# Performance work log

Hardware: AMD Instinct MI355X
Metric: run time of the kernel (lower is better)

The kernel has to match this reference:

```python
import jax, jax.numpy as jnp
import numpy as np

NUM_CLASSES = 100
QUEUE_SIZE = 256
FEATURE_DIM = 1024
BATCH = 4096
EPS = 1e-12  # torch F.normalize eps


def _l2norm(x):
    n = jnp.linalg.norm(x, axis=-1, keepdims=True)
    return x / jnp.maximum(n, EPS)


def setup_inputs() -> dict:
    key = jax.random.key(0)
    k1, k2, k3, k4 = jax.random.split(key, 4)
    embeddings = jax.random.normal(k1, (BATCH, FEATURE_DIM), dtype=jnp.float32)
    labels = jax.random.randint(k2, (BATCH,), 0, NUM_CLASSES, dtype=jnp.int64)
    # buffer initialized as randn then L2-normalized (as in __init__)
    queue = _l2norm(jax.random.normal(k3, (NUM_CLASSES, QUEUE_SIZE, FEATURE_DIM), dtype=jnp.float32))
    queue_ptr = jax.random.randint(k4, (NUM_CLASSES,), 0, QUEUE_SIZE, dtype=jnp.int64)
    return {"embeddings": embeddings, "labels": labels, "queue": queue, "queue_ptr": queue_ptr}


def reference(embeddings, labels, queue, queue_ptr):
    # MemoryBank.update with tail_classes=None: store_idx == label.
    # Serial FIFO semantics: the k-th occurrence of class c in the batch is
    # written at slot (queue_ptr[c] + k) % queue_size.
    queue_size = queue.shape[1]
    emb = _l2norm(embeddings.astype(jnp.float32))  # (B, d)
    # rank[b] = number of earlier batch elements with the same label
    same = labels[:, None] == labels[None, :]           # (B, B)
    rank = jnp.sum(jnp.tril(same, k=-1), axis=1)        # (B,)
    slots = (queue_ptr[labels] + rank) % queue_size      # (B,)
    new_queue = queue.at[labels, slots].set(emb)
    return new_queue
```

## Files before the change

### kernel.cpp

```cpp
#include <hip/hip_runtime.h>

#define NUM_CLASSES 100
#define QUEUE_SIZE  256
#define FEATURE_DIM 1024
#define BATCH       4096
#define TOTAL_ROWS  (NUM_CLASSES * QUEUE_SIZE)
#define EPS         1e-12f

typedef float f32x4 __attribute__((ext_vector_type(4)));

__global__ __launch_bounds__(256) void compute_slots_kernel(
    const int* __restrict__ labels,
    const int* __restrict__ queue_ptr,
    int* __restrict__ inv)
{
    __shared__ int hist[NUM_CLASSES];
    __shared__ int s_lab[256];

    const int tid = threadIdx.x;
    const int chunk_start = blockIdx.x * 256;

    for (int i = tid; i < NUM_CLASSES; i += 256) hist[i] = 0;
    __syncthreads();

    for (int j = tid; j < chunk_start; j += 256) {
        atomicAdd(&hist[labels[j]], 1);
    }
    s_lab[tid] = labels[chunk_start + tid];
    __syncthreads();

    const int lab = s_lab[tid];
    int rank = hist[lab];
    for (int j = 0; j < tid; ++j) {
        rank += (s_lab[j] == lab) ? 1 : 0;
    }
    const int slot = (queue_ptr[lab] + rank) & (QUEUE_SIZE - 1);
    const int row  = lab * QUEUE_SIZE + slot;
    const int b    = chunk_start + tid;
    atomicMax(&inv[row], b);
}

__global__ __launch_bounds__(256) void fused_write_kernel(
    const float* __restrict__ queue,
    const float* __restrict__ emb,
    const int* __restrict__ inv,
    float* __restrict__ out)
{
    const int row = blockIdx.x;
    const int tid = threadIdx.x;
    const long base = (long)row * FEATURE_DIM;

    const int b = inv[row];

    if (b < 0) {
        const f32x4* src = reinterpret_cast<const f32x4*>(queue + base);
        f32x4*       dst = reinterpret_cast<f32x4*>(out + base);
        f32x4 v = __builtin_nontemporal_load(&src[tid]);
        __builtin_nontemporal_store(v, &dst[tid]);
        return;
    }

    const f32x4* src = reinterpret_cast<const f32x4*>(emb + (long)b * FEATURE_DIM);
    f32x4 v = src[tid];

    float ss = v.x * v.x + v.y * v.y + v.z * v.z + v.w * v.w;
    #pragma unroll
    for (int off = 32; off > 0; off >>= 1) {
        ss += __shfl_down(ss, off, 64);
    }

    __shared__ float s_part[4];
    const int lane = tid & 63;
    const int wave = tid >> 6;
    if (lane == 0) s_part[wave] = ss;
    __syncthreads();

    const float total = s_part[0] + s_part[1] + s_part[2] + s_part[3];
    const float inv_n = 1.0f / fmaxf(sqrtf(total), EPS);

    f32x4 o = v * inv_n;

    f32x4* dst = reinterpret_cast<f32x4*>(out + base);
    __builtin_nontemporal_store(o, &dst[tid]);
}

extern "C" void kernel_launch(void* const* d_in, const int* in_sizes, int n_in,
                              void* d_out, int out_size, void* d_ws, size_t ws_size,
                              hipStream_t stream)
{
    const float* embeddings = (const float*)d_in[0];
    const int*   labels     = (const int*)d_in[1];
    const float* queue      = (const float*)d_in[2];
    const int*   queue_ptr  = (const int*)d_in[3];

    float* out = (float*)d_out;
    int*   inv = (int*)d_ws;

    (void)hipMemsetAsync(inv, 0xFF, TOTAL_ROWS * sizeof(int), stream);

    compute_slots_kernel<<<BATCH / 256, 256, 0, stream>>>(labels, queue_ptr, inv);

    fused_write_kernel<<<TOTAL_ROWS, 256, 0, stream>>>(queue, embeddings, inv, out);
}
```

Before: 47.73 us.

## Precompute embedding norms in prep kernel and process eight rows per block

The per-row inverse norm computation moves into the slot-computing kernel, which gains extra blocks where each wave reduces one embedding row into a scale buffer in workspace. The write kernel then handles eight output rows per block with no reduction or barrier on the data path, issuing all eight loads before the stores to raise memory-level parallelism. This cuts block count eightfold and drops the per-row shared-memory reduction. The cost is an extra full read of the embeddings (16 MB) in the prep kernel, and the nontemporal load on queue rows is lost.

```diff
diff --git a/kernel.cpp b/kernel.cpp
--- a/kernel.cpp
+++ b/kernel.cpp
@@ -6,82 +6,101 @@
 #define BATCH       4096
 #define TOTAL_ROWS  (NUM_CLASSES * QUEUE_SIZE)
 #define EPS         1e-12f
+#define ROWS_PER_BLOCK 8
+#define SLOT_BLOCKS (BATCH / 256)
+#define NORM_BLOCKS (BATCH / 4)
 
 typedef float f32x4 __attribute__((ext_vector_type(4)));
 
-__global__ __launch_bounds__(256) void compute_slots_kernel(
+__global__ __launch_bounds__(256) void prep_kernel(
+    const float* __restrict__ emb,
     const int* __restrict__ labels,
     const int* __restrict__ queue_ptr,
-    int* __restrict__ inv)
+    int* __restrict__ inv,
+    float* __restrict__ scale)
 {
-    __shared__ int hist[NUM_CLASSES];
-    __shared__ int s_lab[256];
+    if (blockIdx.x < SLOT_BLOCKS) {
+        __shared__ int hist[NUM_CLASSES];
+        __shared__ int s_lab[256];
 
-    const int tid = threadIdx.x;
-    const int chunk_start = blockIdx.x * 256;
+        const int tid = threadIdx.x;
+        const int chunk_start = blockIdx.x * 256;
 
-    for (int i = tid; i < NUM_CLASSES; i += 256) hist[i] = 0;
-    __syncthreads();
+        for (int i = tid; i < NUM_CLASSES; i += 256) hist[i] = 0;
+        __syncthreads();
 
-    for (int j = tid; j < chunk_start; j += 256) {
-        atomicAdd(&hist[labels[j]], 1);
+        for (int j = tid; j < chunk_start; j += 256) {
+            atomicAdd(&hist[labels[j]], 1);
+        }
+        s_lab[tid] = labels[chunk_start + tid];
+        __syncthreads();
+
+        const int lab = s_lab[tid];
+        int rank = hist[lab];
+        for (int j = 0; j < tid; ++j) {
+            rank += (s_lab[j] == lab) ? 1 : 0;
+        }
+        const int slot = (queue_ptr[lab] + rank) & (QUEUE_SIZE - 1);
+        const int row  = lab * QUEUE_SIZE + slot;
+        atomicMax(&inv[row], chunk_start + tid);
+    } else {
+        const int tid  = threadIdx.x;
+        const int wave = tid >> 6;
+        const int lane = tid & 63;
+        const int b = (blockIdx.x - SLOT_BLOCKS) * 4 + wave;
+
+        const f32x4* src = reinterpret_cast<const f32x4*>(emb + (long)b * FEATURE_DIM);
+        float ss = 0.0f;
+        #pragma unroll
+        for (int it = 0; it < 4; ++it) {
+            f32x4 v = src[it * 64 + lane];
+            ss += v.x * v.x + v.y * v.y + v.z * v.z + v.w * v.w;
+        }
+        #pragma unroll
+        for (int off = 32; off; off >>= 1) {
+            ss += __shfl_xor(ss, off, 64);
+        }
+        if (lane == 0) {
+            scale[b] = 1.0f / fmaxf(sqrtf(ss), EPS);
+        }
     }
-    s_lab[tid] = labels[chunk_start + tid];
-    __syncthreads();
-
-    const int lab = s_lab[tid];
-    int rank = hist[lab];
-    for (int j = 0; j < tid; ++j) {
-        rank += (s_lab[j] == lab) ? 1 : 0;
-    }
-    const int slot = (queue_ptr[lab] + rank) & (QUEUE_SIZE - 1);
-    const int row  = lab * QUEUE_SIZE + slot;
-    const int b    = chunk_start + tid;
-    atomicMax(&inv[row], b);
 }
 
 __global__ __launch_bounds__(256) void fused_write_kernel(
     const float* __restrict__ queue,
     const float* __restrict__ emb,
     const int* __restrict__ inv,
+    const float* __restrict__ scale,
     float* __restrict__ out)
 {
-    const int row = blockIdx.x;
-    const int tid = threadIdx.x;
-    const long base = (long)row * FEATURE_DIM;
+    const int tid  = threadIdx.x;
+    const int row0 = blockIdx.x * ROWS_PER_BLOCK;
 
-    const int b = inv[row];
+    __shared__ int   s_b[ROWS_PER_BLOCK];
+    __shared__ float s_s[ROWS_PER_BLOCK];
+    if (tid < ROWS_PER_BLOCK) {
+        const int b = inv[row0 + tid];
+        s_b[tid] = b;
+        s_s[tid] = (b < 0) ? 1.0f : scale[b];
+    }
+    __syncthreads();
 
-    if (b < 0) {
-        const f32x4* src = reinterpret_cast<const f32x4*>(queue + base);
-        f32x4*       dst = reinterpret_cast<f32x4*>(out + base);
-        f32x4 v = __builtin_nontemporal_load(&src[tid]);
-        __builtin_nontemporal_store(v, &dst[tid]);
-        return;
+    f32x4 v[ROWS_PER_BLOCK];
+    #pragma unroll
+    for (int i = 0; i < ROWS_PER_BLOCK; ++i) {
+        const int b = s_b[i];
+        const f32x4* src = (b < 0)
+            ? reinterpret_cast<const f32x4*>(queue + (long)(row0 + i) * FEATURE_DIM)
+            : reinterpret_cast<const f32x4*>(emb + (long)b * FEATURE_DIM);
+        v[i] = src[tid];
     }
 
-    const f32x4* src = reinterpret_cast<const f32x4*>(emb + (long)b * FEATURE_DIM);
-    f32x4 v = src[tid];
-
-    float ss = v.x * v.x + v.y * v.y + v.z * v.z + v.w * v.w;
     #pragma unroll
-    for (int off = 32; off > 0; off >>= 1) {
-        ss += __shfl_down(ss, off, 64);
+    for (int i = 0; i < ROWS_PER_BLOCK; ++i) {
+        f32x4 o = v[i] * s_s[i];
+        f32x4* dst = reinterpret_cast<f32x4*>(out + (long)(row0 + i) * FEATURE_DIM);
+        __builtin_nontemporal_store(o, &dst[tid]);
     }
-
-    __shared__ float s_part[4];
-    const int lane = tid & 63;
-    const int wave = tid >> 6;
-    if (lane == 0) s_part[wave] = ss;
-    __syncthreads();
-
-    const float total = s_part[0] + s_part[1] + s_part[2] + s_part[3];
-    const float inv_n = 1.0f / fmaxf(sqrtf(total), EPS);
-
-    f32x4 o = v * inv_n;
-
-    f32x4* dst = reinterpret_cast<f32x4*>(out + base);
-    __builtin_nontemporal_store(o, &dst[tid]);
 }
 
 extern "C" void kernel_launch(void* const* d_in, const int* in_sizes, int n_in,
@@ -93,12 +112,15 @@
     const float* queue      = (const float*)d_in[2];
     const int*   queue_ptr  = (const int*)d_in[3];
 
-    float* out = (float*)d_out;
-    int*   inv = (int*)d_ws;
+    float* out   = (float*)d_out;
+    int*   inv   = (int*)d_ws;
+    float* scale = (float*)((char*)d_ws + TOTAL_ROWS * sizeof(int));
 
     (void)hipMemsetAsync(inv, 0xFF, TOTAL_ROWS * sizeof(int), stream);
 
-    compute_slots_kernel<<<BATCH / 256, 256, 0, stream>>>(labels, queue_ptr, inv);
+    prep_kernel<<<SLOT_BLOCKS + NORM_BLOCKS, 256, 0, stream>>>(
+        embeddings, labels, queue_ptr, inv, scale);
 
-    fused_write_kernel<<<TOTAL_ROWS, 256, 0, stream>>>(queue, embeddings, inv, out);
+    fused_write_kernel<<<TOTAL_ROWS / ROWS_PER_BLOCK, 256, 0, stream>>>(
+        queue, embeddings, inv, scale, out);
 }
```

After: 50.87 us. +6.6%, slower.

## Map one row per wavefront in fused write kernel, removing block sync

Applied to the files above, without the earlier changes.

Restructures the write kernel so each 64-lane wavefront handles a whole 1024-float row with four vector loads, and each block covers four rows. The L2 norm reduction becomes a wave-local xor shuffle, with no shared memory or __syncthreads. Queue copies switch from nontemporal loads to plain loads. The aim is to cut the block count and barrier overhead and to give each thread more memory operations in flight. The cost is more registers per thread and fewer blocks.

```diff
diff --git a/kernel.cpp b/kernel.cpp
--- a/kernel.cpp
+++ b/kernel.cpp
@@ -36,8 +36,7 @@
     }
     const int slot = (queue_ptr[lab] + rank) & (QUEUE_SIZE - 1);
     const int row  = lab * QUEUE_SIZE + slot;
-    const int b    = chunk_start + tid;
-    atomicMax(&inv[row], b);
+    atomicMax(&inv[row], chunk_start + tid);
 }
 
 __global__ __launch_bounds__(256) void fused_write_kernel(
@@ -46,42 +45,47 @@
     const int* __restrict__ inv,
     float* __restrict__ out)
 {
-    const int row = blockIdx.x;
-    const int tid = threadIdx.x;
+    const int tid  = threadIdx.x;
+    const int lane = tid & 63;
+    const int wave = tid >> 6;
+    const int row  = blockIdx.x * 4 + wave;
     const long base = (long)row * FEATURE_DIM;
 
     const int b = inv[row];
+    f32x4* dst = reinterpret_cast<f32x4*>(out + base);
 
     if (b < 0) {
         const f32x4* src = reinterpret_cast<const f32x4*>(queue + base);
-        f32x4*       dst = reinterpret_cast<f32x4*>(out + base);
-        f32x4 v = __builtin_nontemporal_load(&src[tid]);
-        __builtin_nontemporal_store(v, &dst[tid]);
-        return;
+        f32x4 v0 = src[lane];
+        f32x4 v1 = src[lane + 64];
+        f32x4 v2 = src[lane + 128];
+        f32x4 v3 = src[lane + 192];
+        __builtin_nontemporal_store(v0, &dst[lane]);
+        __builtin_nontemporal_store(v1, &dst[lane + 64]);
+        __builtin_nontemporal_store(v2, &dst[lane + 128]);
+        __builtin_nontemporal_store(v3, &dst[lane + 192]);
+    } else {
+        const f32x4* src = reinterpret_cast<const f32x4*>(emb + (long)b * FEATURE_DIM);
+        f32x4 v0 = src[lane];
+        f32x4 v1 = src[lane + 64];
+        f32x4 v2 = src[lane + 128];
+        f32x4 v3 = src[lane + 192];
+
+        float ss = v0.x*v0.x + v0.y*v0.y + v0.z*v0.z + v0.w*v0.w
+                 + v1.x*v1.x + v1.y*v1.y + v1.z*v1.z + v1.w*v1.w
+                 + v2.x*v2.x + v2.y*v2.y + v2.z*v2.z + v2.w*v2.w
+                 + v3.x*v3.x + v3.y*v3.y + v3.z*v3.z + v3.w*v3.w;
+        #pragma unroll
+        for (int off = 32; off; off >>= 1) {
+            ss += __shfl_xor(ss, off, 64);
+        }
+        const float s = 1.0f / fmaxf(sqrtf(ss), EPS);
+
+        __builtin_nontemporal_store(v0 * s, &dst[lane]);
+        __builtin_nontemporal_store(v1 * s, &dst[lane + 64]);
+        __builtin_nontemporal_store(v2 * s, &dst[lane + 128]);
+        __builtin_nontemporal_store(v3 * s, &dst[lane + 192]);
     }
-
-    const f32x4* src = reinterpret_cast<const f32x4*>(emb + (long)b * FEATURE_DIM);
-    f32x4 v = src[tid];
-
-    float ss = v.x * v.x + v.y * v.y + v.z * v.z + v.w * v.w;
-    #pragma unroll
-    for (int off = 32; off > 0; off >>= 1) {
-        ss += __shfl_down(ss, off, 64);
-    }
-
-    __shared__ float s_part[4];
-    const int lane = tid & 63;
-    const int wave = tid >> 6;
-    if (lane == 0) s_part[wave] = ss;
-    __syncthreads();
-
-    const float total = s_part[0] + s_part[1] + s_part[2] + s_part[3];
-    const float inv_n = 1.0f / fmaxf(sqrtf(total), EPS);
-
-    f32x4 o = v * inv_n;
-
-    f32x4* dst = reinterpret_cast<f32x4*>(out + base);
-    __builtin_nontemporal_store(o, &dst[tid]);
 }
 
 extern "C" void kernel_launch(void* const* d_in, const int* in_sizes, int n_in,
@@ -100,5 +104,6 @@
 
     compute_slots_kernel<<<BATCH / 256, 256, 0, stream>>>(labels, queue_ptr, inv);
 
-    fused_write_kernel<<<TOTAL_ROWS, 256, 0, stream>>>(queue, embeddings, inv, out);
+    fused_write_kernel<<<TOTAL_ROWS / 4, 256, 0, stream>>>(
+        queue, embeddings, inv, out);
 }
```

Measured after the change: 48.76 us. 1.02x slower.

## Process two rows per wavefront with branchless source select in write kernel

Applied to the files above, without the earlier changes.

Restructures the copy/normalize kernel so each 64-lane wave handles two full rows, with four 16-byte loads per lane per row, instead of one block of 256 threads per row. The per-row branch becomes a pointer select, and the block-level shared-memory reduction and __syncthreads are replaced by wave-local xor shuffles. This cuts the block count by 8x and raises memory-level parallelism per thread, at the cost of more registers. Queue rows now also pay for a sum-of-squares reduction whose result is thrown away.

```diff
diff --git a/kernel.cpp b/kernel.cpp
--- a/kernel.cpp
+++ b/kernel.cpp
@@ -36,8 +36,7 @@
     }
     const int slot = (queue_ptr[lab] + rank) & (QUEUE_SIZE - 1);
     const int row  = lab * QUEUE_SIZE + slot;
-    const int b    = chunk_start + tid;
-    atomicMax(&inv[row], b);
+    atomicMax(&inv[row], chunk_start + tid);
 }
 
 __global__ __launch_bounds__(256) void fused_write_kernel(
@@ -46,42 +45,57 @@
     const int* __restrict__ inv,
     float* __restrict__ out)
 {
-    const int row = blockIdx.x;
-    const int tid = threadIdx.x;
-    const long base = (long)row * FEATURE_DIM;
-
-    const int b = inv[row];
-
-    if (b < 0) {
-        const f32x4* src = reinterpret_cast<const f32x4*>(queue + base);
-        f32x4*       dst = reinterpret_cast<f32x4*>(out + base);
-        f32x4 v = __builtin_nontemporal_load(&src[tid]);
-        __builtin_nontemporal_store(v, &dst[tid]);
-        return;
-    }
-
-    const f32x4* src = reinterpret_cast<const f32x4*>(emb + (long)b * FEATURE_DIM);
-    f32x4 v = src[tid];
-
-    float ss = v.x * v.x + v.y * v.y + v.z * v.z + v.w * v.w;
-    #pragma unroll
-    for (int off = 32; off > 0; off >>= 1) {
-        ss += __shfl_down(ss, off, 64);
-    }
-
-    __shared__ float s_part[4];
+    const int tid  = threadIdx.x;
     const int lane = tid & 63;
     const int wave = tid >> 6;
-    if (lane == 0) s_part[wave] = ss;
-    __syncthreads();
+    const int row0 = blockIdx.x * 8 + wave * 2;
+    const int row1 = row0 + 1;
+    const long base0 = (long)row0 * FEATURE_DIM;
+    const long base1 = (long)row1 * FEATURE_DIM;
 
-    const float total = s_part[0] + s_part[1] + s_part[2] + s_part[3];
-    const float inv_n = 1.0f / fmaxf(sqrtf(total), EPS);
+    const int b0 = inv[row0];
+    const int b1 = inv[row1];
 
-    f32x4 o = v * inv_n;
+    const f32x4* s0 = reinterpret_cast<const f32x4*>(
+        (b0 < 0) ? (queue + base0) : (emb + (long)b0 * FEATURE_DIM));
+    const f32x4* s1 = reinterpret_cast<const f32x4*>(
+        (b1 < 0) ? (queue + base1) : (emb + (long)b1 * FEATURE_DIM));
 
-    f32x4* dst = reinterpret_cast<f32x4*>(out + base);
-    __builtin_nontemporal_store(o, &dst[tid]);
+    f32x4 a0 = __builtin_nontemporal_load(&s0[lane]);
+    f32x4 a1 = __builtin_nontemporal_load(&s0[lane + 64]);
+    f32x4 a2 = __builtin_nontemporal_load(&s0[lane + 128]);
+    f32x4 a3 = __builtin_nontemporal_load(&s0[lane + 192]);
+    f32x4 c0 = __builtin_nontemporal_load(&s1[lane]);
+    f32x4 c1 = __builtin_nontemporal_load(&s1[lane + 64]);
+    f32x4 c2 = __builtin_nontemporal_load(&s1[lane + 128]);
+    f32x4 c3 = __builtin_nontemporal_load(&s1[lane + 192]);
+
+    float ssa = a0.x*a0.x + a0.y*a0.y + a0.z*a0.z + a0.w*a0.w
+              + a1.x*a1.x + a1.y*a1.y + a1.z*a1.z + a1.w*a1.w
+              + a2.x*a2.x + a2.y*a2.y + a2.z*a2.z + a2.w*a2.w
+              + a3.x*a3.x + a3.y*a3.y + a3.z*a3.z + a3.w*a3.w;
+    float ssc = c0.x*c0.x + c0.y*c0.y + c0.z*c0.z + c0.w*c0.w
+              + c1.x*c1.x + c1.y*c1.y + c1.z*c1.z + c1.w*c1.w
+              + c2.x*c2.x + c2.y*c2.y + c2.z*c2.z + c2.w*c2.w
+              + c3.x*c3.x + c3.y*c3.y + c3.z*c3.z + c3.w*c3.w;
+    #pragma unroll
+    for (int off = 32; off; off >>= 1) {
+        ssa += __shfl_xor(ssa, off, 64);
+        ssc += __shfl_xor(ssc, off, 64);
+    }
+    const float sc0 = (b0 < 0) ? 1.0f : 1.0f / fmaxf(sqrtf(ssa), EPS);
+    const float sc1 = (b1 < 0) ? 1.0f : 1.0f / fmaxf(sqrtf(ssc), EPS);
+
+    f32x4* d0 = reinterpret_cast<f32x4*>(out + base0);
+    f32x4* d1 = reinterpret_cast<f32x4*>(out + base1);
+    __builtin_nontemporal_store(a0 * sc0, &d0[lane]);
+    __builtin_nontemporal_store(a1 * sc0, &d0[lane + 64]);
+    __builtin_nontemporal_store(a2 * sc0, &d0[lane + 128]);
+    __builtin_nontemporal_store(a3 * sc0, &d0[lane + 192]);
+    __builtin_nontemporal_store(c0 * sc1, &d1[lane]);
+    __builtin_nontemporal_store(c1 * sc1, &d1[lane + 64]);
+    __builtin_nontemporal_store(c2 * sc1, &d1[lane + 128]);
+    __builtin_nontemporal_store(c3 * sc1, &d1[lane + 192]);
 }
 
 extern "C" void kernel_launch(void* const* d_in, const int* in_sizes, int n_in,
@@ -100,5 +114,6 @@
 
     compute_slots_kernel<<<BATCH / 256, 256, 0, stream>>>(labels, queue_ptr, inv);
 
-    fused_write_kernel<<<TOTAL_ROWS, 256, 0, stream>>>(queue, embeddings, inv, out);
+    fused_write_kernel<<<TOTAL_ROWS / 8, 256, 0, stream>>>(
+        queue, embeddings, inv, out);
 }
```

New measurement: 49.50 us. 3.7% more time.
